# Performance work log

Hardware: AMD Instinct MI355X
Metric: run time of the kernel (lower is better)

Reference implementation:

```python
import jax, jax.numpy as jnp
import numpy as np
import math

DEGREE = 3
N_FEATURES = 16
BATCH = 262144
N_POLY = math.comb(N_FEATURES + DEGREE, DEGREE)  # 969


def _poly(x, degree):
    """Polynomial features up to `degree`, matching TaylorMap._poly ordering.

    Uses the Pascal-triangle column counts: for degree block d, feature i is
    multiplied against the first comb(d-1+i, d-1) columns of the previous block.
    Loops are over fixed degree/feature counts (unrolled at trace time).
    """
    n = x.shape[-1]
    b = x.shape[0]
    blocks = [jnp.ones((b, 1), x.dtype), x]
    for d in range(2, degree + 1):
        counts = [math.comb(d - 1 + j, d - 1) for j in range(n)]  # pascal row d-1
        last = blocks[-1]
        blocks.append(
            jnp.concatenate(
                [x[:, i : i + 1] * last[:, :m] for i, m in enumerate(counts)],
                axis=-1,
            )
        )
    return jnp.concatenate(blocks, axis=-1)  # [b, comb(n+degree, degree)]


def setup_inputs() -> dict:
    key = jax.random.key(0)
    kx, kw = jax.random.split(key)
    x = jax.random.normal(kx, (BATCH, N_FEATURES), dtype=jnp.float32)
    # W initialized small so the residual map stays well-conditioned
    W = jax.random.normal(kw, (N_POLY, N_FEATURES), dtype=jnp.float32) * 0.01
    return {"x": x, "W": W}


def reference(x, W):
    """TaylorMap forward: x + poly(x) @ W."""
    return x + _poly(x, DEGREE) @ W
```

## Files before the change

### kernel.cpp

```cpp
#include <hip/hip_runtime.h>

#define NSTEP 39
#define NCOL  (NSTEP * 8)

typedef _Float16 half8   __attribute__((ext_vector_type(8)));
typedef __fp16   f16x2   __attribute__((ext_vector_type(2)));
typedef __fp16   f16x4   __attribute__((ext_vector_type(4)));
typedef __fp16   f16x8   __attribute__((ext_vector_type(8)));
typedef float    float4v __attribute__((ext_vector_type(4)));

struct Cols { short mode[NCOL]; short a[NCOL]; short b[NCOL]; short o[NCOL]; };
static constexpr Cols mk_cols() {
  Cols c{};
  int k = 0;
  for (int o = 0; o < 16; o += 4) { c.mode[k] = 1; c.o[k] = (short)o; ++k; }
  c.mode[k] = 4; ++k;
  for (int a = 0; a < 16; ++a)
    for (int o = 0; o <= a; o += 4) { c.mode[k] = 2; c.a[k] = (short)a; c.o[k] = (short)o; ++k; }
  for (int a = 0; a < 16; ++a)
    for (int b = 0; b <= a; ++b)
      for (int o = (a & ~3); o < 16; o += 4) {
        c.mode[k] = 3; c.a[k] = (short)a; c.b[k] = (short)b; c.o[k] = (short)o; ++k;
      }
  for (; k < NCOL; ++k) c.mode[k] = 0;
  return c;
}
static constexpr Cols COLS = mk_cols();

__global__ void build_wfrag(const float* __restrict__ W, _Float16* __restrict__ Wp) {
  const int e = blockIdx.x * 256 + threadIdx.x;
  if (e >= NSTEP * 64) return;
  const int step = e >> 6;
  const int q    = (e >> 4) & 3;
  const int n    = e & 15;
  half8 hv;
  #pragma unroll
  for (int j = 0; j < 8; ++j) {
    const int c = step * 8 + j;
    const int mode = COLS.mode[c], a = COLS.a[c], b = COLS.b[c], o = COLS.o[c];
    float v = 0.0f;
    if (mode == 3) {
      const int i = o + q;
      if (i >= a) v = W[(153 + i * (i + 1) * (i + 2) / 6 + a * (a + 1) / 2 + b) * 16 + n];
    } else if (mode == 2) {
      const int bb = o + q;
      if (bb <= a) v = W[(17 + a * (a + 1) / 2 + bb) * 16 + n];
    } else if (mode == 1) {
      const int i = o + q;
      v = W[(1 + i) * 16 + n];
      if (i == n) v += 1.0f;
    } else if (mode == 4) {
      if (q == 0) v = W[n];
    }
    hv[j] = (_Float16)v;
  }
  *(half8*)(Wp + e * 8) = hv;
}

template<int C>
__device__ __forceinline__ float colval(const float (&xr)[16], const float (&w4)[4]) {
  if constexpr (COLS.mode[C] == 3)      return (xr[COLS.a[C]] * xr[COLS.b[C]]) * w4[COLS.o[C] >> 2];
  else if constexpr (COLS.mode[C] == 2) return xr[COLS.a[C]] * w4[COLS.o[C] >> 2];
  else if constexpr (COLS.mode[C] == 1) return w4[COLS.o[C] >> 2];
  else if constexpr (COLS.mode[C] == 4) return 1.0f;
  else                                  return 0.0f;
}

template<int Q>
__device__ __forceinline__ void setw4(const float (&xr)[2][16], float (&w4)[2][4]) {
  #pragma unroll
  for (int t = 0; t < 2; ++t)
    #pragma unroll
    for (int j = 0; j < 4; ++j)
      w4[t][j] = xr[t][4 * j + Q];
}

template<int S>
__device__ __forceinline__ void steps(const _Float16* __restrict__ wfq,
                                      const float (&xr)[2][16], const float (&w4)[2][4],
                                      float4v (&acc)[2]) {
  if constexpr (S < NSTEP) {
    const half8 bf = *(const half8*)(wfq + S * 512);
    #pragma unroll
    for (int t = 0; t < 2; ++t) {
      const f16x2 p01 = __builtin_amdgcn_cvt_pkrtz(colval<S * 8 + 0>(xr[t], w4[t]),
                                                   colval<S * 8 + 1>(xr[t], w4[t]));
      const f16x2 p23 = __builtin_amdgcn_cvt_pkrtz(colval<S * 8 + 2>(xr[t], w4[t]),
                                                   colval<S * 8 + 3>(xr[t], w4[t]));
      const f16x2 p45 = __builtin_amdgcn_cvt_pkrtz(colval<S * 8 + 4>(xr[t], w4[t]),
                                                   colval<S * 8 + 5>(xr[t], w4[t]));
      const f16x2 p67 = __builtin_amdgcn_cvt_pkrtz(colval<S * 8 + 6>(xr[t], w4[t]),
                                                   colval<S * 8 + 7>(xr[t], w4[t]));
      const f16x4 lo = __builtin_shufflevector(p01, p23, 0, 1, 2, 3);
      const f16x4 hi = __builtin_shufflevector(p45, p67, 0, 1, 2, 3);
      const f16x8 a8 = __builtin_shufflevector(lo, hi, 0, 1, 2, 3, 4, 5, 6, 7);
      const half8 af = __builtin_bit_cast(half8, a8);
      acc[t] = __builtin_amdgcn_mfma_f32_16x16x32_f16(af, bf, acc[t], 0, 0, 0);
    }
    steps<S + 1>(wfq, xr, w4, acc);
  }
}

__global__ __launch_bounds__(512, 6)
void taylor_fwd(const float* __restrict__ X, const _Float16* __restrict__ Wp,
                float* __restrict__ O) {
  __shared__ _Float16 wfrag[NSTEP * 512];
  const int tid  = threadIdx.x;
  const int lane = tid & 63;
  const int wv   = tid >> 6;
  const int m    = lane & 15;
  const int q    = lane >> 4;

  {
    float4v* dst = (float4v*)wfrag;
    const float4v* src = (const float4v*)Wp;
    #pragma unroll
    for (int i = 0; i < 5; ++i) {
      const int idx = tid + i * 512;
      if (idx < NSTEP * 64) dst[idx] = src[idx];
    }
  }
  __syncthreads();

  const int rb = blockIdx.x * 256 + wv * 32;
  float xr[2][16];
  #pragma unroll
  for (int t = 0; t < 2; ++t) {
    const float4v* xp = (const float4v*)(X + (size_t)(rb + t * 16 + m) * 16);
    #pragma unroll
    for (int c4 = 0; c4 < 4; ++c4) {
      const float4v v = xp[c4];
      xr[t][c4 * 4 + 0] = v[0]; xr[t][c4 * 4 + 1] = v[1];
      xr[t][c4 * 4 + 2] = v[2]; xr[t][c4 * 4 + 3] = v[3];
    }
  }

  float w4[2][4];
  if (q == 0)      setw4<0>(xr, w4);
  else if (q == 1) setw4<1>(xr, w4);
  else if (q == 2) setw4<2>(xr, w4);
  else             setw4<3>(xr, w4);

  float4v acc[2];
  acc[0] = (float4v){0.f, 0.f, 0.f, 0.f};
  acc[1] = (float4v){0.f, 0.f, 0.f, 0.f};

  const _Float16* wfq = wfrag + (q * 16 + m) * 8;
  steps<0>(wfq, xr, w4, acc);

  #pragma unroll
  for (int t = 0; t < 2; ++t) {
    #pragma unroll
    for (int r = 0; r < 4; ++r) {
      const int row = rb + t * 16 + q * 4 + r;
      O[(size_t)row * 16 + m] = acc[t][r];
    }
  }
}

extern "C" void kernel_launch(void* const* d_in, const int* in_sizes, int n_in,
                              void* d_out, int out_size, void* d_ws, size_t ws_size,
                              hipStream_t stream) {
  const float* X = (const float*)d_in[0];
  const float* W = (const float*)d_in[1];
  float*       O = (float*)d_out;
  _Float16*    Wp = (_Float16*)d_ws;
  const int batch = in_sizes[0] / 16;
  const int grid  = batch / 256;

  build_wfrag<<<(NSTEP * 64 + 255) / 256, 256, 0, stream>>>(W, Wp);
  taylor_fwd<<<grid, 512, 0, stream>>>(X, Wp, O);
}
```

Before: 89.94 us.

## Compute polynomial features with packed fp16 math and pair-friendly column order

The polynomial feature columns are reordered so that adjacent column pairs share one operand structure. Each pair is then produced by a single packed fp16 multiply chain on inputs converted to half once at load, instead of fp32 multiplies followed by a pack-convert for every pair of columns. This is meant to roughly halve the vector-ALU work that feeds the MFMA instructions, which looks like the bottleneck here. The launch bound is also raised to 8 blocks per multiprocessor, which caps register use per thread. In exchange, the degree-2 and degree-3 products are now rounded in fp16 at each step rather than once at the end, which loses some accuracy.

```diff
diff --git a/kernel.cpp b/kernel.cpp
--- a/kernel.cpp
+++ b/kernel.cpp
@@ -15,13 +15,20 @@
   int k = 0;
   for (int o = 0; o < 16; o += 4) { c.mode[k] = 1; c.o[k] = (short)o; ++k; }
   c.mode[k] = 4; ++k;
-  for (int a = 0; a < 16; ++a)
-    for (int o = 0; o <= a; o += 4) { c.mode[k] = 2; c.a[k] = (short)a; c.o[k] = (short)o; ++k; }
-  for (int a = 0; a < 16; ++a)
-    for (int b = 0; b <= a; ++b)
-      for (int o = (a & ~3); o < 16; o += 4) {
-        c.mode[k] = 3; c.a[k] = (short)a; c.b[k] = (short)b; c.o[k] = (short)o; ++k;
+  c.mode[k] = 0; ++k;
+  for (int o = 0; o < 16; o += 4)
+    for (int a = o; a < 16; ++a) { c.mode[k] = 2; c.a[k] = (short)a; c.o[k] = (short)o; ++k; }
+  for (int o = 0; o < 16; o += 4) {
+    const int amax = (o + 3 < 15) ? o + 3 : 15;
+    for (int a = 0; a <= amax; ++a)
+      for (int b = 0; b + 1 <= a; b += 2) {
+        c.mode[k] = 3; c.a[k] = (short)a; c.b[k] = (short)b;     c.o[k] = (short)o; ++k;
+        c.mode[k] = 3; c.a[k] = (short)a; c.b[k] = (short)(b+1); c.o[k] = (short)o; ++k;
       }
+    for (int a = 0; a <= amax; a += 2) {
+      c.mode[k] = 3; c.a[k] = (short)a; c.b[k] = (short)a; c.o[k] = (short)o; ++k;
+    }
+  }
   for (; k < NCOL; ++k) c.mode[k] = 0;
   return c;
 }
@@ -58,50 +65,64 @@
 }
 
 template<int C>
-__device__ __forceinline__ float colval(const float (&xr)[16], const float (&w4)[4]) {
-  if constexpr (COLS.mode[C] == 3)      return (xr[COLS.a[C]] * xr[COLS.b[C]]) * w4[COLS.o[C] >> 2];
-  else if constexpr (COLS.mode[C] == 2) return xr[COLS.a[C]] * w4[COLS.o[C] >> 2];
-  else if constexpr (COLS.mode[C] == 1) return w4[COLS.o[C] >> 2];
-  else if constexpr (COLS.mode[C] == 4) return 1.0f;
-  else                                  return 0.0f;
+__device__ __forceinline__ f16x2 colpair(const f16x2 (&x2)[8], const f16x2 (&w2)[4]) {
+  constexpr int m0 = COLS.mode[C], m1 = COLS.mode[C + 1];
+  if constexpr (m0 == 3 && COLS.a[C] == COLS.b[C]) {
+    constexpr int a1 = COLS.a[C], a2 = COLS.a[C + 1];
+    const f16x2 s = __builtin_shufflevector(x2[a1 / 2], x2[a2 / 2], a1 % 2, 2 + a2 % 2);
+    return (s * s) * w2[COLS.o[C] >> 2];
+  } else if constexpr (m0 == 3) {
+    constexpr int a = COLS.a[C], b = COLS.b[C];
+    const f16x2 xa = __builtin_shufflevector(x2[a / 2], x2[a / 2], a % 2, a % 2);
+    return (xa * x2[b / 2]) * w2[COLS.o[C] >> 2];
+  } else if constexpr (m0 == 2) {
+    return x2[COLS.a[C] / 2] * w2[COLS.o[C] >> 2];
+  } else if constexpr (m0 == 1 && m1 == 1) {
+    return __builtin_shufflevector(w2[COLS.o[C] >> 2], w2[COLS.o[C + 1] >> 2], 0, 2);
+  } else if constexpr (m0 == 4) {
+    return (f16x2){(__fp16)1.0f, (__fp16)0.0f};
+  } else {
+    return (f16x2){(__fp16)0.0f, (__fp16)0.0f};
+  }
+}
+
+template<int Q, int T, int J>
+__device__ __forceinline__ void setw2_one(const f16x2 (&x2)[2][8], f16x2 (&w2)[2][4]) {
+  constexpr int idx = 4 * J + Q;
+  w2[T][J] = __builtin_shufflevector(x2[T][idx / 2], x2[T][idx / 2], idx % 2, idx % 2);
 }
 
 template<int Q>
-__device__ __forceinline__ void setw4(const float (&xr)[2][16], float (&w4)[2][4]) {
-  #pragma unroll
-  for (int t = 0; t < 2; ++t)
-    #pragma unroll
-    for (int j = 0; j < 4; ++j)
-      w4[t][j] = xr[t][4 * j + Q];
+__device__ __forceinline__ void setw2(const f16x2 (&x2)[2][8], f16x2 (&w2)[2][4]) {
+  setw2_one<Q, 0, 0>(x2, w2); setw2_one<Q, 0, 1>(x2, w2);
+  setw2_one<Q, 0, 2>(x2, w2); setw2_one<Q, 0, 3>(x2, w2);
+  setw2_one<Q, 1, 0>(x2, w2); setw2_one<Q, 1, 1>(x2, w2);
+  setw2_one<Q, 1, 2>(x2, w2); setw2_one<Q, 1, 3>(x2, w2);
 }
 
 template<int S>
 __device__ __forceinline__ void steps(const _Float16* __restrict__ wfq,
-                                      const float (&xr)[2][16], const float (&w4)[2][4],
+                                      const f16x2 (&x2)[2][8], const f16x2 (&w2)[2][4],
                                       float4v (&acc)[2]) {
   if constexpr (S < NSTEP) {
     const half8 bf = *(const half8*)(wfq + S * 512);
     #pragma unroll
     for (int t = 0; t < 2; ++t) {
-      const f16x2 p01 = __builtin_amdgcn_cvt_pkrtz(colval<S * 8 + 0>(xr[t], w4[t]),
-                                                   colval<S * 8 + 1>(xr[t], w4[t]));
-      const f16x2 p23 = __builtin_amdgcn_cvt_pkrtz(colval<S * 8 + 2>(xr[t], w4[t]),
-                                                   colval<S * 8 + 3>(xr[t], w4[t]));
-      const f16x2 p45 = __builtin_amdgcn_cvt_pkrtz(colval<S * 8 + 4>(xr[t], w4[t]),
-                                                   colval<S * 8 + 5>(xr[t], w4[t]));
-      const f16x2 p67 = __builtin_amdgcn_cvt_pkrtz(colval<S * 8 + 6>(xr[t], w4[t]),
-                                                   colval<S * 8 + 7>(xr[t], w4[t]));
+      const f16x2 p01 = colpair<S * 8 + 0>(x2[t], w2[t]);
+      const f16x2 p23 = colpair<S * 8 + 2>(x2[t], w2[t]);
+      const f16x2 p45 = colpair<S * 8 + 4>(x2[t], w2[t]);
+      const f16x2 p67 = colpair<S * 8 + 6>(x2[t], w2[t]);
       const f16x4 lo = __builtin_shufflevector(p01, p23, 0, 1, 2, 3);
       const f16x4 hi = __builtin_shufflevector(p45, p67, 0, 1, 2, 3);
       const f16x8 a8 = __builtin_shufflevector(lo, hi, 0, 1, 2, 3, 4, 5, 6, 7);
       const half8 af = __builtin_bit_cast(half8, a8);
       acc[t] = __builtin_amdgcn_mfma_f32_16x16x32_f16(af, bf, acc[t], 0, 0, 0);
     }
-    steps<S + 1>(wfq, xr, w4, acc);
+    steps<S + 1>(wfq, x2, w2, acc);
   }
 }
 
-__global__ __launch_bounds__(512, 6)
+__global__ __launch_bounds__(512, 8)
 void taylor_fwd(const float* __restrict__ X, const _Float16* __restrict__ Wp,
                 float* __restrict__ O) {
   __shared__ _Float16 wfrag[NSTEP * 512];
@@ -123,30 +144,30 @@
   __syncthreads();
 
   const int rb = blockIdx.x * 256 + wv * 32;
-  float xr[2][16];
+  f16x2 x2[2][8];
   #pragma unroll
   for (int t = 0; t < 2; ++t) {
     const float4v* xp = (const float4v*)(X + (size_t)(rb + t * 16 + m) * 16);
     #pragma unroll
     for (int c4 = 0; c4 < 4; ++c4) {
       const float4v v = xp[c4];
-      xr[t][c4 * 4 + 0] = v[0]; xr[t][c4 * 4 + 1] = v[1];
-      xr[t][c4 * 4 + 2] = v[2]; xr[t][c4 * 4 + 3] = v[3];
+      x2[t][c4 * 2 + 0] = __builtin_amdgcn_cvt_pkrtz(v[0], v[1]);
+      x2[t][c4 * 2 + 1] = __builtin_amdgcn_cvt_pkrtz(v[2], v[3]);
     }
   }
 
-  float w4[2][4];
-  if (q == 0)      setw4<0>(xr, w4);
-  else if (q == 1) setw4<1>(xr, w4);
-  else if (q == 2) setw4<2>(xr, w4);
-  else             setw4<3>(xr, w4);
+  f16x2 w2[2][4];
+  if (q == 0)      setw2<0>(x2, w2);
+  else if (q == 1) setw2<1>(x2, w2);
+  else if (q == 2) setw2<2>(x2, w2);
+  else             setw2<3>(x2, w2);
 
   float4v acc[2];
   acc[0] = (float4v){0.f, 0.f, 0.f, 0.f};
   acc[1] = (float4v){0.f, 0.f, 0.f, 0.f};
 
   const _Float16* wfq = wfrag + (q * 16 + m) * 8;
-  steps<0>(wfq, xr, w4, acc);
+  steps<0>(wfq, x2, w2, acc);
 
   #pragma unroll
   for (int t = 0; t < 2; ++t) {
```

Measured after the change: 108.7 us. +20.9%, slower.
